# Performance work log

Hardware: AMD Instinct MI355X
Metric: run time of the kernel (lower is better)

Reference implementation:

```python
import jax, jax.numpy as jnp
import numpy as np
from jax import lax

# Quantization bit-widths per the module: QuantAct(16) on input,
# QuantConv2d(precision[0]=8), QuantAct(precision[0]+3=11) after relu1,
# QuantLinear(precision[1]=8).
INPUT_BIT = 16
CONV_W_BIT = 8
RELU_BIT = 11
DENSE_W_BIT = 8
EPS = 1e-8


def round_ste(x):
    # straight-through estimator rounding (HAWQ SymmetricQuantFunction)
    return x + lax.stop_gradient(jnp.round(x) - x)


def quant_act(x, bit):
    """Per-tensor symmetric dynamic activation quantization (HAWQ QuantAct).
    Returns fake-quantized x and its scaling factor."""
    n = 2 ** (bit - 1) - 1
    scale = lax.stop_gradient(jnp.maximum(jnp.max(jnp.abs(x)), EPS) / n)
    x_q = jnp.clip(round_ste(x / scale), -n, n) * scale
    return x_q, scale


def quant_weight(w, bit):
    """Per-output-channel symmetric weight quantization. w: [out, ...].
    Returns integer-valued weights and per-channel scale [out]."""
    n = 2 ** (bit - 1) - 1
    absmax = jnp.max(jnp.abs(w.reshape(w.shape[0], -1)), axis=1)
    sf = lax.stop_gradient(jnp.maximum(absmax, EPS) / n)
    bshape = (w.shape[0],) + (1,) * (w.ndim - 1)
    w_int = jnp.clip(round_ste(w / sf.reshape(bshape)), -n, n)
    return w_int, sf


def quant_conv2d(x, p_sf, w, b, bit, stride, pad):
    w_int, w_sf = quant_weight(w, bit)          # [O,I,kh,kw], [O]
    x_int = x / p_sf                            # integer-valued activations
    out_int = lax.conv_general_dilated(
        x_int, w_int, window_strides=(stride, stride),
        padding=((pad, pad), (pad, pad)),
        dimension_numbers=("NCHW", "OIHW", "NCHW"))
    bias_sf = p_sf * w_sf                       # [O]
    b_int = round_ste(b / bias_sf)
    out = (out_int + b_int[None, :, None, None]) * bias_sf[None, :, None, None]
    return out, w_sf


def quant_linear(x, p_sf, w, b, bit):
    w_int, w_sf = quant_weight(w, bit)          # [O,I], [O]
    x_int = x / p_sf
    bias_sf = p_sf * w_sf                       # [O]
    b_int = round_ste(b / bias_sf)
    out = (jnp.einsum("bi,oi->bo", x_int, w_int) + b_int[None, :]) * bias_sf[None, :]
    return out


def setup_inputs() -> dict:
    key = jax.random.key(0)
    k1, k2, k3, k4, k5 = jax.random.split(key, 5)
    B, Cin, H, W = 256, 3, 64, 64
    Cout, K = 64, 3
    Fin, Fout = Cout * 32 * 32, 256  # stride-2 conv -> 32x32 spatial
    x = jax.random.normal(k1, (B, Cin, H, W), dtype=jnp.float32)
    conv_w = jax.random.normal(k2, (Cout, Cin, K, K), dtype=jnp.float32) * 0.1
    conv_b = jax.random.normal(k3, (Cout,), dtype=jnp.float32) * 0.01
    dense_w = jax.random.normal(k4, (Fout, Fin), dtype=jnp.float32) * 0.02
    dense_b = jax.random.normal(k5, (Fout,), dtype=jnp.float32) * 0.01
    return {"x": x, "conv_w": conv_w, "conv_b": conv_b,
            "dense_w": dense_w, "dense_b": dense_b}


def reference(x, conv_w, conv_b, dense_w, dense_b):
    # x, p_sf = quant_input(x)
    xq, p_sf = quant_act(x, INPUT_BIT)
    # x, w_sf = conv(x, p_sf)
    h, w_sf = quant_conv2d(xq, p_sf, conv_w, conv_b, CONV_W_BIT, stride=2, pad=1)
    # relu1
    h = jax.nn.relu(h)
    # x, p_sf = quant_relu(x, p_sf, w_sf)  (requantize at relu_bit)
    h, p_sf = quant_act(h, RELU_BIT)
    # flatten
    h = h.reshape(h.shape[0], -1)
    # relu2(enc_dense(x, p_sf))
    out = jax.nn.relu(quant_linear(h, p_sf, dense_w, dense_b, DENSE_W_BIT))
    return out
```

## Files before the change

kernel.cpp:

```cpp
#include <hip/hip_runtime.h>
#include <hip/hip_fp16.h>
#include <cstdint>

#define B_   256
#define CIN  3
#define HW_  64
#define COUT 64
#define FIN  65536
#define FOUT 256

#define ACC_F    0
#define SC_F     65536
#define WSF2_F   65552
#define CBSF_F   65808
#define CBINT_F  65872
#define CWINT_F  65936
#define H16_BYTE (512*1024)

typedef _Float16 half8  __attribute__((ext_vector_type(8)));
typedef _Float16 half4v __attribute__((ext_vector_type(4)));
typedef float    floatx4 __attribute__((ext_vector_type(4)));
typedef unsigned short u16;

__device__ inline float blockMax(float v) {
    #pragma unroll
    for (int off = 32; off; off >>= 1) v = fmaxf(v, __shfl_down(v, off));
    __shared__ float sm[8];
    const int lane = threadIdx.x & 63, w = threadIdx.x >> 6;
    if (lane == 0) sm[w] = v;
    __syncthreads();
    float m = sm[0];
    const int nw = blockDim.x >> 6;
    for (int i = 1; i < nw; i++) m = fmaxf(m, sm[i]);
    return m;
}

__global__ void k_amax_x(const float* __restrict__ x, unsigned* __restrict__ tgt, int n4) {
    const float4* x4 = (const float4*)x;
    float m = 0.f;
    for (int i = blockIdx.x * blockDim.x + threadIdx.x; i < n4; i += gridDim.x * blockDim.x) {
        float4 v = x4[i];
        m = fmaxf(m, fmaxf(fmaxf(fabsf(v.x), fabsf(v.y)), fmaxf(fabsf(v.z), fabsf(v.w))));
    }
    float bm = blockMax(m);
    if (threadIdx.x == 0) atomicMax(tgt, __float_as_uint(bm));
}

__global__ void k_wamax(const float* __restrict__ dw, unsigned* __restrict__ wabs) {
    const int row = blockIdx.x >> 2;
    const int q   = blockIdx.x & 3;
    const float4* r = (const float4*)(dw + (size_t)row * FIN) + q * 4096;
    float m = 0.f;
    for (int i = threadIdx.x; i < 4096; i += 256) {
        float4 v = r[i];
        m = fmaxf(m, fmaxf(fmaxf(fabsf(v.x), fabsf(v.y)), fmaxf(fabsf(v.z), fabsf(v.w))));
    }
    float bm = blockMax(m);
    if (threadIdx.x == 0) atomicMax(wabs + row, __float_as_uint(bm));
}

__global__ void k_qconvw(const float* __restrict__ cw, const float* __restrict__ cb,
                         float* ws) {
    const int o = threadIdx.x;
    const float maxx = __uint_as_float(((const unsigned*)ws)[SC_F + 0]);
    const float p_sf = fmaxf(maxx, 1e-8f) / 32767.0f;
    if (o == 0) ws[SC_F + 2] = p_sf;
    float wv[27];
    float m = 0.f;
    #pragma unroll
    for (int i = 0; i < 27; i++) { wv[i] = cw[o * 27 + i]; m = fmaxf(m, fabsf(wv[i])); }
    const float sf = fmaxf(m, 1e-8f) / 127.0f;
    #pragma unroll
    for (int i = 0; i < 27; i++) {
        float qv = fminf(127.f, fmaxf(-127.f, rintf(wv[i] / sf)));
        ws[CWINT_F + o * 27 + i] = qv;
    }
    const float bsf = p_sf * sf;
    ws[CBSF_F + o]  = bsf;
    ws[CBINT_F + o] = rintf(cb[o] / bsf);
}

__global__ __launch_bounds__(256) void k_conv(const float* __restrict__ x,
                                              const float* __restrict__ ws,
                                              u16* __restrict__ h16,
                                              unsigned* __restrict__ maxh) {
    const int b   = blockIdx.x >> 3;
    const int oyt = (blockIdx.x & 7) * 4;
    const int t   = threadIdx.x;
    const int ox  = t & 31;
    const int ch  = __builtin_amdgcn_readfirstlane((t >> 6) & 1);
    const int oy  = oyt + ((t >> 7) << 1) + ((t >> 5) & 1);
    const float p_sf  = ws[SC_F + 2];
    const float inv_p = 1.0f / p_sf;
    const float* xb = x + (size_t)b * (CIN * HW_ * HW_);

    float xs[27];
    #pragma unroll
    for (int ci = 0; ci < 3; ci++)
        #pragma unroll
        for (int ky = 0; ky < 3; ky++) {
            const int iy = 2 * oy - 1 + ky;
            const bool yok = ((unsigned)iy < 64u);
            #pragma unroll
            for (int kx = 0; kx < 3; kx++) {
                const int ix = 2 * ox - 1 + kx;
                float v = (yok && ((unsigned)ix < 64u)) ? xb[(ci * HW_ + iy) * HW_ + ix] : 0.f;
                float q = rintf(v * inv_p);
                xs[ci * 9 + ky * 3 + kx] = fminf(32767.f, fmaxf(-32767.f, q));
            }
        }

    float acc[32];
    const float* wr = ws + CWINT_F + ch * (32 * 27);
    #pragma unroll
    for (int c = 0; c < 32; c++) {
        float a = 0.f;
        #pragma unroll
        for (int k = 0; k < 27; k++) a = fmaf(xs[k], wr[c * 27 + k], a);
        acc[c] = a;
    }

    float mx = 0.f;
    const size_t base = (size_t)b * FIN + (size_t)ch * 32 * 1024 + oy * 32 + ox;
    #pragma unroll
    for (int c = 0; c < 32; c++) {
        const int co = ch * 32 + c;
        float h = (acc[c] + ws[CBINT_F + co]) * ws[CBSF_F + co];
        h = fmaxf(h, 0.f);
        mx = fmaxf(mx, h);
        h16[base + (size_t)c * 1024] = __half_as_ushort(__float2half(h));
    }
    float bm = blockMax(mx);
    if (t == 0) atomicMax(maxh, __float_as_uint(bm));
}

__global__ __launch_bounds__(256) void k_gemm(const u16* __restrict__ h16,
                                              const float* __restrict__ dw,
                                              const float* __restrict__ ws,
                                              float* __restrict__ accb) {
    __shared__ __align__(16) _Float16 As[128][72];
    __shared__ __align__(16) _Float16 Bs[128][72];
    __shared__ float invB[128];

    const int tid = threadIdx.x;
    const int tm  = (blockIdx.x >> 1) * 128;
    const int tn  = (blockIdx.x & 1) * 128;
    const int k0  = blockIdx.y * 1024;

    const float max_h  = __uint_as_float(((const unsigned*)ws)[SC_F + 1]);
    const float p2     = fmaxf(max_h, 1e-8f) / 1023.0f;
    const float inv_p2 = 1.0f / p2;

    if (tid < 128) {
        float am = fmaxf(__uint_as_float(((const unsigned*)ws)[WSF2_F + tn + tid]), 1e-8f);
        invB[tid] = 127.0f / am;
    }

    floatx4 acc[4][4];
    const floatx4 zz = {0.f, 0.f, 0.f, 0.f};
    #pragma unroll
    for (int i = 0; i < 4; i++)
        #pragma unroll
        for (int j = 0; j < 4; j++) acc[i][j] = zz;

    const int wv = tid >> 6, lane = tid & 63;
    const int wm = (wv >> 1) * 64, wn = (wv & 1) * 64;
    const int lm = lane & 15, quad = lane >> 4;

    for (int kk = 0; kk < 16; kk++) {
        __syncthreads();
        #pragma unroll
        for (int r = 0; r < 4; r++) {
            const int i = tid + r * 256;
            const int row = i >> 3, c = i & 7;
            const u16* p = h16 + (size_t)(tm + row) * FIN + k0 + kk * 64 + c * 8;
            half8 hv = *(const half8*)p;
            half8 qv;
            #pragma unroll
            for (int j = 0; j < 8; j++) {
                float f = (float)hv[j];
                qv[j] = (_Float16)fminf(1023.f, rintf(f * inv_p2));
            }
            *(half8*)&As[row][c * 8] = qv;
        }
        #pragma unroll
        for (int r = 0; r < 8; r++) {
            const int i = tid + r * 256;
            const int row = i >> 4, c = i & 15;
            const float* p = dw + (size_t)(tn + row) * FIN + k0 + kk * 64 + c * 4;
            float4 v = *(const float4*)p;
            const float is = invB[row];
            half4v qv;
            qv[0] = (_Float16)fminf(127.f, fmaxf(-127.f, rintf(v.x * is)));
            qv[1] = (_Float16)fminf(127.f, fmaxf(-127.f, rintf(v.y * is)));
            qv[2] = (_Float16)fminf(127.f, fmaxf(-127.f, rintf(v.z * is)));
            qv[3] = (_Float16)fminf(127.f, fmaxf(-127.f, rintf(v.w * is)));
            *(half4v*)&Bs[row][c * 4] = qv;
        }
        __syncthreads();
        #pragma unroll
        for (int ks = 0; ks < 2; ks++) {
            half8 af[4], bf[4];
            #pragma unroll
            for (int mi = 0; mi < 4; mi++)
                af[mi] = *(const half8*)&As[wm + mi * 16 + lm][ks * 32 + quad * 8];
            #pragma unroll
            for (int ni = 0; ni < 4; ni++)
                bf[ni] = *(const half8*)&Bs[wn + ni * 16 + lm][ks * 32 + quad * 8];
            #pragma unroll
            for (int mi = 0; mi < 4; mi++)
                #pragma unroll
                for (int ni = 0; ni < 4; ni++)
                    acc[mi][ni] = __builtin_amdgcn_mfma_f32_16x16x32_f16(af[mi], bf[ni], acc[mi][ni], 0, 0, 0);
        }
    }

    #pragma unroll
    for (int mi = 0; mi < 4; mi++)
        #pragma unroll
        for (int ni = 0; ni < 4; ni++)
            #pragma unroll
            for (int r = 0; r < 4; r++) {
                const int row = tm + wm + mi * 16 + quad * 4 + r;
                const int col = tn + wn + ni * 16 + lm;
                atomicAdd(accb + row * FOUT + col, acc[mi][ni][r]);
            }
}

__global__ void k_epi(const float* __restrict__ accb, const float* __restrict__ db,
                      const float* __restrict__ ws, float* __restrict__ out) {
    const int idx = blockIdx.x * 256 + threadIdx.x;
    const int n = idx & 255;
    const float max_h = __uint_as_float(((const unsigned*)ws)[SC_F + 1]);
    const float p2 = fmaxf(max_h, 1e-8f) / 1023.0f;
    const float am = fmaxf(__uint_as_float(((const unsigned*)ws)[WSF2_F + n]), 1e-8f);
    const float wsf = am / 127.0f;
    const float bsf = p2 * wsf;
    const float bint = rintf(db[n] / bsf);
    out[idx] = fmaxf(0.f, (accb[idx] + bint) * bsf);
}

extern "C" void kernel_launch(void* const* d_in, const int* in_sizes, int n_in,
                              void* d_out, int out_size, void* d_ws, size_t ws_size,
                              hipStream_t stream) {
    (void)in_sizes; (void)n_in; (void)out_size; (void)ws_size;
    const float* x  = (const float*)d_in[0];
    const float* cw = (const float*)d_in[1];
    const float* cb = (const float*)d_in[2];
    const float* dw = (const float*)d_in[3];
    const float* db = (const float*)d_in[4];
    float* out = (float*)d_out;
    float* ws  = (float*)d_ws;
    u16* h16   = (u16*)((char*)d_ws + H16_BYTE);
    float* accb = ws + ACC_F;
    unsigned* scal = (unsigned*)(ws + SC_F);
    unsigned* wabs = (unsigned*)(ws + WSF2_F);

    hipMemsetAsync(d_ws, 0, (size_t)(65536 + 16 + 256) * sizeof(float), stream);

    k_amax_x<<<512, 256, 0, stream>>>(x, scal + 0, (B_ * CIN * HW_ * HW_) / 4);
    k_wamax<<<1024, 256, 0, stream>>>(dw, wabs);
    k_qconvw<<<1, 64, 0, stream>>>(cw, cb, ws);
    k_conv<<<2048, 256, 0, stream>>>(x, ws, h16, scal + 1);
    k_gemm<<<dim3(4, 64), 256, 0, stream>>>(h16, dw, ws, accb);
    k_epi<<<256, 256, 0, stream>>>(accb, db, ws, out);
}
```

Measured before the change: 207.6 us.

## Pre-quantize dense weights to int8 and register-prefetch GEMM tiles

Merges the two absmax kernels into one launch. Adds a kernel that quantizes the dense weights once to packed int8 in the workspace, so the GEMM reads 1 byte per weight instead of 4 and each M-tile no longer re-reads and re-quantizes fp32 weights. The GEMM doubles split-K (K chunk 512, grid 4x128) and prefetches the next A/B tile into registers while MFMAs run, with an extra barrier per iteration. The cost is an extra full pass over the 64 MB fp32 weight matrix plus a 16 MB int8 write, and more atomic adds into the split-K accumulator.

```diff
diff --git a/kernel.cpp b/kernel.cpp
--- a/kernel.cpp
+++ b/kernel.cpp
@@ -16,9 +16,9 @@
 #define CBINT_F  65872
 #define CWINT_F  65936
 #define H16_BYTE (512*1024)
+#define WQ_BYTE  (36*1024*1024)
 
 typedef _Float16 half8  __attribute__((ext_vector_type(8)));
-typedef _Float16 half4v __attribute__((ext_vector_type(4)));
 typedef float    floatx4 __attribute__((ext_vector_type(4)));
 typedef unsigned short u16;
 
@@ -35,28 +35,29 @@
     return m;
 }
 
-__global__ void k_amax_x(const float* __restrict__ x, unsigned* __restrict__ tgt, int n4) {
-    const float4* x4 = (const float4*)x;
-    float m = 0.f;
-    for (int i = blockIdx.x * blockDim.x + threadIdx.x; i < n4; i += gridDim.x * blockDim.x) {
-        float4 v = x4[i];
-        m = fmaxf(m, fmaxf(fmaxf(fabsf(v.x), fabsf(v.y)), fmaxf(fabsf(v.z), fabsf(v.w))));
-    }
-    float bm = blockMax(m);
-    if (threadIdx.x == 0) atomicMax(tgt, __float_as_uint(bm));
-}
-
-__global__ void k_wamax(const float* __restrict__ dw, unsigned* __restrict__ wabs) {
-    const int row = blockIdx.x >> 2;
-    const int q   = blockIdx.x & 3;
-    const float4* r = (const float4*)(dw + (size_t)row * FIN) + q * 4096;
-    float m = 0.f;
-    for (int i = threadIdx.x; i < 4096; i += 256) {
-        float4 v = r[i];
-        m = fmaxf(m, fmaxf(fmaxf(fabsf(v.x), fabsf(v.y)), fmaxf(fabsf(v.z), fabsf(v.w))));
-    }
-    float bm = blockMax(m);
-    if (threadIdx.x == 0) atomicMax(wabs + row, __float_as_uint(bm));
+__global__ void k_amax(const float* __restrict__ x, const float* __restrict__ dw,
+                       unsigned* __restrict__ scal, unsigned* __restrict__ wabs, int n4x) {
+    if (blockIdx.x < 512) {
+        const float4* x4 = (const float4*)x;
+        float m = 0.f;
+        for (int i = blockIdx.x * blockDim.x + threadIdx.x; i < n4x; i += 512 * 256) {
+            float4 v = x4[i];
+            m = fmaxf(m, fmaxf(fmaxf(fabsf(v.x), fabsf(v.y)), fmaxf(fabsf(v.z), fabsf(v.w))));
+        }
+        float bm = blockMax(m);
+        if (threadIdx.x == 0) atomicMax(scal, __float_as_uint(bm));
+    } else {
+        const int wb = blockIdx.x - 512;
+        const int row = wb >> 2, q = wb & 3;
+        const float4* r = (const float4*)(dw + (size_t)row * FIN) + q * 4096;
+        float m = 0.f;
+        for (int i = threadIdx.x; i < 4096; i += 256) {
+            float4 v = r[i];
+            m = fmaxf(m, fmaxf(fmaxf(fabsf(v.x), fabsf(v.y)), fmaxf(fabsf(v.z), fabsf(v.w))));
+        }
+        float bm = blockMax(m);
+        if (threadIdx.x == 0) atomicMax(wabs + row, __float_as_uint(bm));
+    }
 }
 
 __global__ void k_qconvw(const float* __restrict__ cw, const float* __restrict__ cb,
@@ -78,6 +79,33 @@
     const float bsf = p_sf * sf;
     ws[CBSF_F + o]  = bsf;
     ws[CBINT_F + o] = rintf(cb[o] / bsf);
+}
+
+__global__ __launch_bounds__(256) void k_wquant(const float* __restrict__ dw,
+                                                const float* __restrict__ ws,
+                                                char* __restrict__ wq) {
+    const int gid = blockIdx.x * 256 + threadIdx.x;
+    const int row = gid >> 13;
+    const int c0  = (gid & 8191) * 8;
+    const float am = fmaxf(__uint_as_float(((const unsigned*)ws)[WSF2_F + row]), 1e-8f);
+    const float is = 127.0f / am;
+    const float* p = dw + (size_t)row * FIN + c0;
+    float4 a = *(const float4*)p;
+    float4 b = *(const float4*)(p + 4);
+    float v[8] = {a.x, a.y, a.z, a.w, b.x, b.y, b.z, b.w};
+    unsigned lo = 0, hi = 0;
+    #pragma unroll
+    for (int j = 0; j < 4; j++) {
+        int q = (int)fminf(127.f, fmaxf(-127.f, rintf(v[j] * is)));
+        lo |= ((unsigned)(q & 0xff)) << (8 * j);
+    }
+    #pragma unroll
+    for (int j = 0; j < 4; j++) {
+        int q = (int)fminf(127.f, fmaxf(-127.f, rintf(v[4 + j] * is)));
+        hi |= ((unsigned)(q & 0xff)) << (8 * j);
+    }
+    uint2 out; out.x = lo; out.y = hi;
+    *(uint2*)(wq + (size_t)row * FIN + c0) = out;
 }
 
 __global__ __launch_bounds__(256) void k_conv(const float* __restrict__ x,
@@ -134,28 +162,29 @@
     if (t == 0) atomicMax(maxh, __float_as_uint(bm));
 }
 
+__device__ inline void unpack4(int w, _Float16* d) {
+    d[0] = (_Float16)((w << 24) >> 24);
+    d[1] = (_Float16)((w << 16) >> 24);
+    d[2] = (_Float16)((w << 8) >> 24);
+    d[3] = (_Float16)(w >> 24);
+}
+
 __global__ __launch_bounds__(256) void k_gemm(const u16* __restrict__ h16,
-                                              const float* __restrict__ dw,
+                                              const char* __restrict__ wq,
                                               const float* __restrict__ ws,
                                               float* __restrict__ accb) {
     __shared__ __align__(16) _Float16 As[128][72];
     __shared__ __align__(16) _Float16 Bs[128][72];
-    __shared__ float invB[128];
 
     const int tid = threadIdx.x;
     const int tm  = (blockIdx.x >> 1) * 128;
     const int tn  = (blockIdx.x & 1) * 128;
-    const int k0  = blockIdx.y * 1024;
+    const int k0  = blockIdx.y * 512;
 
     const float max_h  = __uint_as_float(((const unsigned*)ws)[SC_F + 1]);
     const float p2     = fmaxf(max_h, 1e-8f) / 1023.0f;
     const float inv_p2 = 1.0f / p2;
 
-    if (tid < 128) {
-        float am = fmaxf(__uint_as_float(((const unsigned*)ws)[WSF2_F + tn + tid]), 1e-8f);
-        invB[tid] = 127.0f / am;
-    }
-
     floatx4 acc[4][4];
     const floatx4 zz = {0.f, 0.f, 0.f, 0.f};
     #pragma unroll
@@ -167,37 +196,48 @@
     const int wm = (wv >> 1) * 64, wn = (wv & 1) * 64;
     const int lm = lane & 15, quad = lane >> 4;
 
-    for (int kk = 0; kk < 16; kk++) {
-        __syncthreads();
+    const int arow = tid >> 3, ac = tid & 7;
+    const int brow = tid >> 2, bc = tid & 3;
+
+    half8 Ar[4];
+    int4  Br[2];
+
+    auto loadA = [&](int kk) {
+        #pragma unroll
+        for (int r = 0; r < 4; r++)
+            Ar[r] = *(const half8*)(h16 + (size_t)(tm + arow + r * 32) * FIN + k0 + kk * 64 + ac * 8);
+    };
+    auto loadB = [&](int kk) {
+        #pragma unroll
+        for (int r = 0; r < 2; r++)
+            Br[r] = *(const int4*)(wq + (size_t)(tn + brow + r * 64) * FIN + k0 + kk * 64 + bc * 16);
+    };
+
+    loadA(0); loadB(0);
+
+    for (int kk = 0; kk < 8; kk++) {
         #pragma unroll
         for (int r = 0; r < 4; r++) {
-            const int i = tid + r * 256;
-            const int row = i >> 3, c = i & 7;
-            const u16* p = h16 + (size_t)(tm + row) * FIN + k0 + kk * 64 + c * 8;
-            half8 hv = *(const half8*)p;
             half8 qv;
             #pragma unroll
             for (int j = 0; j < 8; j++) {
-                float f = (float)hv[j];
+                float f = (float)Ar[r][j];
                 qv[j] = (_Float16)fminf(1023.f, rintf(f * inv_p2));
             }
-            *(half8*)&As[row][c * 8] = qv;
-        }
-        #pragma unroll
-        for (int r = 0; r < 8; r++) {
-            const int i = tid + r * 256;
-            const int row = i >> 4, c = i & 15;
-            const float* p = dw + (size_t)(tn + row) * FIN + k0 + kk * 64 + c * 4;
-            float4 v = *(const float4*)p;
-            const float is = invB[row];
-            half4v qv;
-            qv[0] = (_Float16)fminf(127.f, fmaxf(-127.f, rintf(v.x * is)));
-            qv[1] = (_Float16)fminf(127.f, fmaxf(-127.f, rintf(v.y * is)));
-            qv[2] = (_Float16)fminf(127.f, fmaxf(-127.f, rintf(v.z * is)));
-            qv[3] = (_Float16)fminf(127.f, fmaxf(-127.f, rintf(v.w * is)));
-            *(half4v*)&Bs[row][c * 4] = qv;
+            *(half8*)&As[arow + r * 32][ac * 8] = qv;
+        }
+        #pragma unroll
+        for (int r = 0; r < 2; r++) {
+            half8 q0, q1;
+            unpack4(Br[r].x, (_Float16*)&q0);
+            unpack4(Br[r].y, ((_Float16*)&q0) + 4);
+            unpack4(Br[r].z, (_Float16*)&q1);
+            unpack4(Br[r].w, ((_Float16*)&q1) + 4);
+            *(half8*)&Bs[brow + r * 64][bc * 16]     = q0;
+            *(half8*)&Bs[brow + r * 64][bc * 16 + 8] = q1;
         }
         __syncthreads();
+        if (kk < 7) { loadA(kk + 1); loadB(kk + 1); }
         #pragma unroll
         for (int ks = 0; ks < 2; ks++) {
             half8 af[4], bf[4];
@@ -213,6 +253,7 @@
                 for (int ni = 0; ni < 4; ni++)
                     acc[mi][ni] = __builtin_amdgcn_mfma_f32_16x16x32_f16(af[mi], bf[ni], acc[mi][ni], 0, 0, 0);
         }
+        __syncthreads();
     }
 
     #pragma unroll
@@ -252,16 +293,17 @@
     float* out = (float*)d_out;
     float* ws  = (float*)d_ws;
     u16* h16   = (u16*)((char*)d_ws + H16_BYTE);
+    char* wq   = (char*)d_ws + WQ_BYTE;
     float* accb = ws + ACC_F;
     unsigned* scal = (unsigned*)(ws + SC_F);
     unsigned* wabs = (unsigned*)(ws + WSF2_F);
 
     hipMemsetAsync(d_ws, 0, (size_t)(65536 + 16 + 256) * sizeof(float), stream);
 
-    k_amax_x<<<512, 256, 0, stream>>>(x, scal + 0, (B_ * CIN * HW_ * HW_) / 4);
-    k_wamax<<<1024, 256, 0, stream>>>(dw, wabs);
+    k_amax<<<1536, 256, 0, stream>>>(x, dw, scal, wabs, (B_ * CIN * HW_ * HW_) / 4);
     k_qconvw<<<1, 64, 0, stream>>>(cw, cb, ws);
+    k_wquant<<<8192, 256, 0, stream>>>(dw, ws, wq);
     k_conv<<<2048, 256, 0, stream>>>(x, ws, h16, scal + 1);
-    k_gemm<<<dim3(4, 64), 256, 0, stream>>>(h16, dw, ws, accb);
+    k_gemm<<<dim3(4, 128), 256, 0, stream>>>(h16, wq, ws, accb);
     k_epi<<<256, 256, 0, stream>>>(accb, db, ws, out);
 }
```

Result: slower. 212.1 us (+2.2%).
